# Optimization experiments

Measured on AMD Instinct MI355X. Metric: run time of the kernel, lower is better.

The kernel has to match this reference:

```python
import jax, jax.numpy as jnp
import numpy as np

N = 32768        # batch of sampled sequences
H = 1024         # LSTM hidden (cell) size
P = 128          # proj_size == output_size == operator_length
IN = 2 * (P + 1) + 4 + 1  # 263 = 2*(operator_length+1) + scatter_max_degree + 1
SOFT = 64        # soft_length
TSS = 16.0       # two_sigma_square
AZB, AZE = 0, 32    # operators.arity_zero_begin/end (token layout assumption)
A2B, A2E = 96, 128  # operators.arity_two_begin/end


def setup_inputs() -> dict:
    key = jax.random.key(0)
    ks = jax.random.split(key, 16)
    s = 0.05
    inp = {
        "input": jax.random.normal(ks[0], (N, IN), jnp.float32),
        "hidden": jax.random.normal(ks[1], (2, N, H), jnp.float32),       # c-state
        "hidden_lstm": jax.random.normal(ks[2], (2, N, P), jnp.float32),  # h-state (proj)
        # layer 0 (input -> H, projected to P)
        "W_ih0": jax.random.normal(ks[3], (4 * H, IN), jnp.float32) * s,
        "W_hh0": jax.random.normal(ks[4], (4 * H, P), jnp.float32) * s,
        "b_ih0": jax.random.normal(ks[5], (4 * H,), jnp.float32) * s,
        "b_hh0": jax.random.normal(ks[6], (4 * H,), jnp.float32) * s,
        "W_hr0": jax.random.normal(ks[7], (P, H), jnp.float32) * s,
        # layer 1 (P -> H, projected to P)
        "W_ih1": jax.random.normal(ks[8], (4 * H, P), jnp.float32) * s,
        "W_hh1": jax.random.normal(ks[9], (4 * H, P), jnp.float32) * s,
        "b_ih1": jax.random.normal(ks[10], (4 * H,), jnp.float32) * s,
        "b_hh1": jax.random.normal(ks[11], (4 * H,), jnp.float32) * s,
        "W_hr1": jax.random.normal(ks[12], (P, H), jnp.float32) * s,
        "cur_length": 10,
    }
    return inp


def lstm_cell(x, h, c, Wih, Whh, bih, bhh, Whr):
    # PyTorch gate order: i, f, g, o ; proj_size projection via Whr
    gates = x @ Wih.T + h @ Whh.T + (bih + bhh)   # [n, 4H]
    i, f, g, o = jnp.split(gates, 4, axis=-1)
    c_new = jax.nn.sigmoid(f) * c + jax.nn.sigmoid(i) * jnp.tanh(g)
    h_new = (jax.nn.sigmoid(o) * jnp.tanh(c_new)) @ Whr.T  # project H -> P
    return h_new, c_new


def reference(input, hidden, hidden_lstm,
              W_ih0, W_hh0, b_ih0, b_hh0, W_hr0,
              W_ih1, W_hh1, b_ih1, b_hh1, W_hr1,
              cur_length):
    h0, c0 = lstm_cell(input, hidden_lstm[0], hidden[0], W_ih0, W_hh0, b_ih0, b_hh0, W_hr0)
    h1, c1 = lstm_cell(h0, hidden_lstm[1], hidden[1], W_ih1, W_hh1, b_ih1, b_hh1, W_hr1)
    # prior bias (cur_length is a static Python int)
    prior = jnp.zeros((P,), jnp.float32)
    if cur_length < SOFT:
        prior = prior.at[AZB:AZE].set(-float(SOFT - cur_length) ** 2 / TSS)
    elif cur_length > SOFT:
        prior = prior.at[A2B:A2E].set(-float(cur_length - SOFT) ** 2 / TSS)
    out = jax.nn.softmax(h1 + prior[None, :], axis=1)  # [n, P]
    cn = jnp.stack([c0, c1])  # [2, n, H]
    hn = jnp.stack([h0, h1])  # [2, n, P]
    return out, cn, hn
```

## Files before the change

### kernel.cpp

```cpp
#include <hip/hip_runtime.h>
#include <stdint.h>

#define NB 32768
#define HH 1024
#define PP 128
#define INW 263
#define K0P 448
#define K1P 256
#define G4H 4096

typedef __attribute__((ext_vector_type(8))) short short8;
typedef __attribute__((ext_vector_type(4))) float floatx4;

__device__ __forceinline__ unsigned short f2bf(float x) {
    union { float f; unsigned int u; } v; v.f = x;
    unsigned int r = v.u + 0x7fffu + ((v.u >> 16) & 1u);
    return (unsigned short)(r >> 16);
}
__device__ __forceinline__ float sigm(float x) { return 1.f / (1.f + __expf(-x)); }
__device__ __forceinline__ float tanhfast(float x) { return 2.f / (1.f + __expf(-2.f * x)) - 1.f; }

__device__ __forceinline__ void load_lds16(const void* g, void* l) {
    __builtin_amdgcn_global_load_lds((const __attribute__((address_space(1))) void*)g,
                                     (__attribute__((address_space(3))) void*)l,
                                     16, 0, 0);
}

__global__ void prep_inputs(const float* __restrict__ inp, const float* __restrict__ hl,
                            unsigned short* __restrict__ X0, unsigned short* __restrict__ X1) {
    const int T0 = NB * K0P;
    const int T1 = T0 + NB * PP;
    for (int idx = blockIdx.x * 256 + threadIdx.x; idx < T1; idx += gridDim.x * 256) {
        if (idx < T0) {
            int n = idx / K0P, c = idx - n * K0P;
            float v = 0.f;
            if (c < INW) v = inp[n * INW + c];
            else if (c < INW + PP) v = hl[n * PP + (c - INW)];
            X0[idx] = f2bf(v);
        } else {
            int k = idx - T0;
            int n = k >> 7, c = k & 127;
            X1[n * K1P + PP + c] = f2bf(hl[NB * PP + k]);
        }
    }
}

__global__ void prep_weights(const float* __restrict__ Wih0, const float* __restrict__ Whh0,
                             const float* __restrict__ Wih1, const float* __restrict__ Whh1,
                             const float* __restrict__ Whr0, const float* __restrict__ Whr1,
                             const float* __restrict__ bih0, const float* __restrict__ bhh0,
                             const float* __restrict__ bih1, const float* __restrict__ bhh1,
                             unsigned short* __restrict__ Wp0, unsigned short* __restrict__ Wp1,
                             unsigned short* __restrict__ Whr0b, unsigned short* __restrict__ Whr1b,
                             float* __restrict__ b0, float* __restrict__ b1) {
    const int T0 = G4H * K0P;
    const int T1 = T0 + G4H * K1P;
    const int T2 = T1 + PP * HH;
    const int T3 = T2 + PP * HH;
    const int T4 = T3 + G4H;
    const int T5 = T4 + G4H;
    for (int idx = blockIdx.x * 256 + threadIdx.x; idx < T5; idx += gridDim.x * 256) {
        if (idx < T0) {
            int r = idx / K0P, c = idx - r * K0P;
            int cbb = r >> 7, tt = r & 127;
            int src = (tt >> 5) * 1024 + cbb * 32 + (tt & 31);
            float v = 0.f;
            if (c < INW) v = Wih0[src * INW + c];
            else if (c < INW + PP) v = Whh0[src * PP + (c - INW)];
            Wp0[idx] = f2bf(v);
        } else if (idx < T1) {
            int k = idx - T0;
            int r = k >> 8, c = k & 255;
            int cbb = r >> 7, tt = r & 127;
            int src = (tt >> 5) * 1024 + cbb * 32 + (tt & 31);
            float v = (c < PP) ? Wih1[src * PP + c] : Whh1[src * PP + (c - PP)];
            Wp1[k] = f2bf(v);
        } else if (idx < T2) {
            int k = idx - T1; Whr0b[k] = f2bf(Whr0[k]);
        } else if (idx < T3) {
            int k = idx - T2; Whr1b[k] = f2bf(Whr1[k]);
        } else if (idx < T4) {
            int k = idx - T3; b0[k] = bih0[k] + bhh0[k];
        } else {
            int k = idx - T4; b1[k] = bih1[k] + bhh1[k];
        }
    }
}

template<int KPAD>
__global__ __launch_bounds__(256, 2) void gemm_gates_k(
    const unsigned short* __restrict__ A,
    const unsigned short* __restrict__ Bp,
    const float* __restrict__ bias,
    const float* __restrict__ c_prev,
    float* __restrict__ c_out,
    unsigned short* __restrict__ tmp_out)
{
    __shared__ unsigned short As[128 * 64];
    __shared__ unsigned short Bs[128 * 64];
    const int t  = threadIdx.x;
    const int w  = t >> 6;
    const int l  = t & 63;
    const int lc = l & 15;
    const int q4 = l >> 4;
    const int cb = blockIdx.x;
    const int mb = blockIdx.y;

    floatx4 acc[2][8];
#pragma unroll
    for (int i = 0; i < 2; ++i)
#pragma unroll
        for (int j = 0; j < 8; ++j) acc[i][j] = (floatx4){0.f, 0.f, 0.f, 0.f};

    const int arow = t >> 3;
    const int sw   = ((t & 7) ^ ((t >> 3) & 7)) * 8;
    const unsigned short* gA = A  + (size_t)(mb * 128 + arow) * KPAD + sw;
    const unsigned short* gB = Bp + (size_t)(cb * 128 + arow) * KPAD + sw;
    char* ldsA = (char*)As + t * 16;
    char* ldsB = (char*)Bs + t * 16;

    for (int kt = 0; kt < KPAD; kt += 64) {
#pragma unroll
        for (int i = 0; i < 4; ++i) {
            load_lds16(gA + (size_t)(i * 32) * KPAD + kt, ldsA + i * 4096);
            load_lds16(gB + (size_t)(i * 32) * KPAD + kt, ldsB + i * 4096);
        }
        __syncthreads();
        const short* Asp = (const short*)As;
        const short* Bsp = (const short*)Bs;
#pragma unroll
        for (int kc = 0; kc < 2; ++kc) {
            const int kchunk = kc * 4 + q4;
            const int rsw = (kchunk ^ (lc & 7)) * 8;
            short8 a[2];
#pragma unroll
            for (int mi = 0; mi < 2; ++mi)
                a[mi] = *(const short8*)&Asp[(w * 32 + mi * 16 + lc) * 64 + rsw];
#pragma unroll
            for (int ci = 0; ci < 8; ++ci) {
                short8 b = *(const short8*)&Bsp[(ci * 16 + lc) * 64 + rsw];
#pragma unroll
                for (int mi = 0; mi < 2; ++mi)
                    acc[mi][ci] = __builtin_amdgcn_mfma_f32_16x16x32_bf16(a[mi], b, acc[mi][ci], 0, 0, 0);
            }
        }
        __syncthreads();
    }

#pragma unroll
    for (int u4 = 0; u4 < 2; ++u4) {
        const int hidx = cb * 32 + u4 * 16 + lc;
        const float bi = bias[hidx];
        const float bf = bias[1024 + hidx];
        const float bg = bias[2048 + hidx];
        const float bo = bias[3072 + hidx];
#pragma unroll
        for (int mi = 0; mi < 2; ++mi) {
#pragma unroll
            for (int r = 0; r < 4; ++r) {
                const int row = mb * 128 + w * 32 + mi * 16 + q4 * 4 + r;
                const float iv = acc[mi][0 + u4][r] + bi;
                const float fv = acc[mi][2 + u4][r] + bf;
                const float gv = acc[mi][4 + u4][r] + bg;
                const float ov = acc[mi][6 + u4][r] + bo;
                const float cp = c_prev[(size_t)row * 1024 + hidx];
                const float cn = sigm(fv) * cp + sigm(iv) * tanhfast(gv);
                c_out[(size_t)row * 1024 + hidx] = cn;
                tmp_out[(size_t)row * 1024 + hidx] = f2bf(sigm(ov) * tanhfast(cn));
            }
        }
    }
}

__global__ __launch_bounds__(256, 2) void gemm_proj_k(
    const unsigned short* __restrict__ A,
    const unsigned short* __restrict__ B,
    float* __restrict__ hout,
    unsigned short* __restrict__ xc1)
{
    __shared__ unsigned short As[128 * 64];
    __shared__ unsigned short Bs[128 * 64];
    const int t  = threadIdx.x;
    const int w  = t >> 6;
    const int l  = t & 63;
    const int lc = l & 15;
    const int q4 = l >> 4;
    const int mb = blockIdx.x;

    floatx4 acc[2][8];
#pragma unroll
    for (int i = 0; i < 2; ++i)
#pragma unroll
        for (int j = 0; j < 8; ++j) acc[i][j] = (floatx4){0.f, 0.f, 0.f, 0.f};

    const int arow = t >> 3;
    const int sw   = ((t & 7) ^ ((t >> 3) & 7)) * 8;
    const unsigned short* gA = A + (size_t)(mb * 128 + arow) * 1024 + sw;
    const unsigned short* gB = B + (size_t)arow * 1024 + sw;
    char* ldsA = (char*)As + t * 16;
    char* ldsB = (char*)Bs + t * 16;

    for (int kt = 0; kt < 1024; kt += 64) {
#pragma unroll
        for (int i = 0; i < 4; ++i) {
            load_lds16(gA + (size_t)(i * 32) * 1024 + kt, ldsA + i * 4096);
            load_lds16(gB + (size_t)(i * 32) * 1024 + kt, ldsB + i * 4096);
        }
        __syncthreads();
        const short* Asp = (const short*)As;
        const short* Bsp = (const short*)Bs;
#pragma unroll
        for (int kc = 0; kc < 2; ++kc) {
            const int kchunk = kc * 4 + q4;
            const int rsw = (kchunk ^ (lc & 7)) * 8;
            short8 a[2];
#pragma unroll
            for (int mi = 0; mi < 2; ++mi)
                a[mi] = *(const short8*)&Asp[(w * 32 + mi * 16 + lc) * 64 + rsw];
#pragma unroll
            for (int ci = 0; ci < 8; ++ci) {
                short8 b = *(const short8*)&Bsp[(ci * 16 + lc) * 64 + rsw];
#pragma unroll
                for (int mi = 0; mi < 2; ++mi)
                    acc[mi][ci] = __builtin_amdgcn_mfma_f32_16x16x32_bf16(a[mi], b, acc[mi][ci], 0, 0, 0);
            }
        }
        __syncthreads();
    }

#pragma unroll
    for (int ci = 0; ci < 8; ++ci) {
        const int col = ci * 16 + lc;
#pragma unroll
        for (int mi = 0; mi < 2; ++mi) {
#pragma unroll
            for (int r = 0; r < 4; ++r) {
                const int row = mb * 128 + w * 32 + mi * 16 + q4 * 4 + r;
                const float v = acc[mi][ci][r];
                hout[(size_t)row * 128 + col] = v;
                if (xc1) xc1[(size_t)row * K1P + col] = f2bf(v);
            }
        }
    }
}

__global__ void softmax_k(const float* __restrict__ h1, const int* __restrict__ clp,
                          float* __restrict__ out) {
    const int w = threadIdx.x >> 6, l = threadIdx.x & 63;
    const int row = blockIdx.x * 4 + w;
    const int cl = clp[0];
    float pd = 0.f;
    float d = (float)(64 - cl);
    float pv = -(d * d) * (1.f / 16.f);
    float p0 = (cl < 64 && l < 32) ? pv : 0.f;
    float p1 = (cl > 64 && (l + 64) >= 96) ? pv : 0.f;
    (void)pd;
    float v0 = h1[(size_t)row * 128 + l] + p0;
    float v1 = h1[(size_t)row * 128 + 64 + l] + p1;
    float m = fmaxf(v0, v1);
#pragma unroll
    for (int off = 32; off > 0; off >>= 1) m = fmaxf(m, __shfl_xor(m, off, 64));
    float e0 = __expf(v0 - m), e1 = __expf(v1 - m);
    float s = e0 + e1;
#pragma unroll
    for (int off = 32; off > 0; off >>= 1) s += __shfl_xor(s, off, 64);
    float inv = 1.f / s;
    out[(size_t)row * 128 + l] = e0 * inv;
    out[(size_t)row * 128 + 64 + l] = e1 * inv;
}

extern "C" void kernel_launch(void* const* d_in, const int* in_sizes, int n_in,
                              void* d_out, int out_size, void* d_ws, size_t ws_size,
                              hipStream_t stream) {
    const float* input = (const float*)d_in[0];
    const float* hidden = (const float*)d_in[1];
    const float* hlstm  = (const float*)d_in[2];
    const float* Wih0 = (const float*)d_in[3];
    const float* Whh0 = (const float*)d_in[4];
    const float* bih0 = (const float*)d_in[5];
    const float* bhh0 = (const float*)d_in[6];
    const float* Whr0 = (const float*)d_in[7];
    const float* Wih1 = (const float*)d_in[8];
    const float* Whh1 = (const float*)d_in[9];
    const float* bih1 = (const float*)d_in[10];
    const float* bhh1 = (const float*)d_in[11];
    const float* Whr1 = (const float*)d_in[12];
    const int* curlen = (const int*)d_in[13];

    float* out = (float*)d_out;
    float* cn0 = out + (size_t)NB * PP;
    float* cn1 = cn0 + (size_t)NB * HH;
    float* hn0 = cn1 + (size_t)NB * HH;
    float* hn1 = hn0 + (size_t)NB * PP;

    char* p = (char*)d_ws;
    unsigned short* X0    = (unsigned short*)p; p += (size_t)NB * K0P * 2;
    unsigned short* X1    = (unsigned short*)p; p += (size_t)NB * K1P * 2;
    unsigned short* Wp0   = (unsigned short*)p; p += (size_t)G4H * K0P * 2;
    unsigned short* Wp1   = (unsigned short*)p; p += (size_t)G4H * K1P * 2;
    unsigned short* Whr0b = (unsigned short*)p; p += (size_t)PP * HH * 2;
    unsigned short* Whr1b = (unsigned short*)p; p += (size_t)PP * HH * 2;
    float* b0 = (float*)p; p += (size_t)G4H * 4;
    float* b1 = (float*)p; p += (size_t)G4H * 4;
    unsigned short* tmp0 = (unsigned short*)p; p += (size_t)NB * HH * 2;
    unsigned short* tmp1 = (unsigned short*)p; p += (size_t)NB * HH * 2;

    prep_inputs<<<8192, 256, 0, stream>>>(input, hlstm, X0, X1);
    prep_weights<<<4096, 256, 0, stream>>>(Wih0, Whh0, Wih1, Whh1, Whr0, Whr1,
                                           bih0, bhh0, bih1, bhh1,
                                           Wp0, Wp1, Whr0b, Whr1b, b0, b1);
    gemm_gates_k<K0P><<<dim3(32, 256), 256, 0, stream>>>(X0, Wp0, b0, hidden, cn0, tmp0);
    gemm_proj_k<<<256, 256, 0, stream>>>(tmp0, Whr0b, hn0, X1);
    gemm_gates_k<K1P><<<dim3(32, 256), 256, 0, stream>>>(X1, Wp1, b1, hidden + (size_t)NB * HH, cn1, tmp1);
    gemm_proj_k<<<256, 256, 0, stream>>>(tmp1, Whr1b, hn1, nullptr);
    softmax_k<<<NB / 4, 256, 0, stream>>>(hn1, curlen, out);
}
```

Baseline: 913.8 us.

## Double-buffer LDS tiles and prefetch c_prev/bias before GEMM main loop

Both GEMM kernels now use two LDS buffers per operand, issuing the global-to-LDS loads for the next K tile before computing the current one. Manual vmcnt waits and raw barriers replace the __syncthreads pairs. The gates kernel also loads c_prev and the bias values into registers before the main loop, hiding their latency behind the MFMA work. This doubles LDS use to 64KB per block, which may limit occupancy at 2 blocks/CU, and adds 40 live registers for the prefetched values.

```diff
diff --git a/kernel.cpp b/kernel.cpp
--- a/kernel.cpp
+++ b/kernel.cpp
@@ -96,8 +96,8 @@
     float* __restrict__ c_out,
     unsigned short* __restrict__ tmp_out)
 {
-    __shared__ unsigned short As[128 * 64];
-    __shared__ unsigned short Bs[128 * 64];
+    __shared__ unsigned short As[2 * 128 * 64];
+    __shared__ unsigned short Bs[2 * 128 * 64];
     const int t  = threadIdx.x;
     const int w  = t >> 6;
     const int l  = t & 63;
@@ -112,22 +112,60 @@
 #pragma unroll
         for (int j = 0; j < 8; ++j) acc[i][j] = (floatx4){0.f, 0.f, 0.f, 0.f};
 
+    float cpv[2][2][4];
+    float bv[2][4];
+#pragma unroll
+    for (int u4 = 0; u4 < 2; ++u4) {
+        const int hidx = cb * 32 + u4 * 16 + lc;
+#pragma unroll
+        for (int j = 0; j < 4; ++j) bv[u4][j] = bias[j * 1024 + hidx];
+#pragma unroll
+        for (int mi = 0; mi < 2; ++mi)
+#pragma unroll
+            for (int r = 0; r < 4; ++r)
+                cpv[u4][mi][r] =
+                    c_prev[(size_t)(mb * 128 + w * 32 + mi * 16 + q4 * 4 + r) * 1024 + hidx];
+    }
+    asm volatile("" ::: "memory");
+
     const int arow = t >> 3;
     const int sw   = ((t & 7) ^ ((t >> 3) & 7)) * 8;
     const unsigned short* gA = A  + (size_t)(mb * 128 + arow) * KPAD + sw;
     const unsigned short* gB = Bp + (size_t)(cb * 128 + arow) * KPAD + sw;
-    char* ldsA = (char*)As + t * 16;
-    char* ldsB = (char*)Bs + t * 16;
-
-    for (int kt = 0; kt < KPAD; kt += 64) {
+
+    constexpr int NT = KPAD / 64;
+
+    {
+        char* lA = (char*)As + t * 16;
+        char* lB = (char*)Bs + t * 16;
 #pragma unroll
         for (int i = 0; i < 4; ++i) {
-            load_lds16(gA + (size_t)(i * 32) * KPAD + kt, ldsA + i * 4096);
-            load_lds16(gB + (size_t)(i * 32) * KPAD + kt, ldsB + i * 4096);
-        }
-        __syncthreads();
-        const short* Asp = (const short*)As;
-        const short* Bsp = (const short*)Bs;
+            load_lds16(gA + (size_t)(i * 32) * KPAD, lA + i * 4096);
+            load_lds16(gB + (size_t)(i * 32) * KPAD, lB + i * 4096);
+        }
+    }
+
+#pragma unroll
+    for (int ki = 0; ki < NT; ++ki) {
+        const int cur = ki & 1;
+        if (ki + 1 < NT) {
+            const int kt = (ki + 1) * 64;
+            char* lA = (char*)As + (cur ^ 1) * 16384 + t * 16;
+            char* lB = (char*)Bs + (cur ^ 1) * 16384 + t * 16;
+#pragma unroll
+            for (int i = 0; i < 4; ++i) {
+                load_lds16(gA + (size_t)(i * 32) * KPAD + kt, lA + i * 4096);
+                load_lds16(gB + (size_t)(i * 32) * KPAD + kt, lB + i * 4096);
+            }
+            asm volatile("s_waitcnt vmcnt(8)" ::: "memory");
+        } else {
+            asm volatile("s_waitcnt vmcnt(0)" ::: "memory");
+        }
+        __builtin_amdgcn_s_barrier();
+        asm volatile("" ::: "memory");
+
+        const short* Asp = (const short*)As + cur * 8192;
+        const short* Bsp = (const short*)Bs + cur * 8192;
 #pragma unroll
         for (int kc = 0; kc < 2; ++kc) {
             const int kchunk = kc * 4 + q4;
@@ -144,16 +182,20 @@
                     acc[mi][ci] = __builtin_amdgcn_mfma_f32_16x16x32_bf16(a[mi], b, acc[mi][ci], 0, 0, 0);
             }
         }
-        __syncthreads();
+        if (ki + 1 < NT) {
+            asm volatile("" ::: "memory");
+            __builtin_amdgcn_s_barrier();
+            asm volatile("" ::: "memory");
+        }
     }
 
 #pragma unroll
     for (int u4 = 0; u4 < 2; ++u4) {
         const int hidx = cb * 32 + u4 * 16 + lc;
-        const float bi = bias[hidx];
-        const float bf = bias[1024 + hidx];
-        const float bg = bias[2048 + hidx];
-        const float bo = bias[3072 + hidx];
+        const float bi = bv[u4][0];
+        const float bf = bv[u4][1];
+        const float bg = bv[u4][2];
+        const float bo = bv[u4][3];
 #pragma unroll
         for (int mi = 0; mi < 2; ++mi) {
 #pragma unroll
@@ -163,7 +205,7 @@
                 const float fv = acc[mi][2 + u4][r] + bf;
                 const float gv = acc[mi][4 + u4][r] + bg;
                 const float ov = acc[mi][6 + u4][r] + bo;
-                const float cp = c_prev[(size_t)row * 1024 + hidx];
+                const float cp = cpv[u4][mi][r];
                 const float cn = sigm(fv) * cp + sigm(iv) * tanhfast(gv);
                 c_out[(size_t)row * 1024 + hidx] = cn;
                 tmp_out[(size_t)row * 1024 + hidx] = f2bf(sigm(ov) * tanhfast(cn));
@@ -178,8 +220,8 @@
     float* __restrict__ hout,
     unsigned short* __restrict__ xc1)
 {
-    __shared__ unsigned short As[128 * 64];
-    __shared__ unsigned short Bs[128 * 64];
+    __shared__ unsigned short As[2 * 128 * 64];
+    __shared__ unsigned short Bs[2 * 128 * 64];
     const int t  = threadIdx.x;
     const int w  = t >> 6;
     const int l  = t & 63;
@@ -197,18 +239,40 @@
     const int sw   = ((t & 7) ^ ((t >> 3) & 7)) * 8;
     const unsigned short* gA = A + (size_t)(mb * 128 + arow) * 1024 + sw;
     const unsigned short* gB = B + (size_t)arow * 1024 + sw;
-    char* ldsA = (char*)As + t * 16;
-    char* ldsB = (char*)Bs + t * 16;
-
-    for (int kt = 0; kt < 1024; kt += 64) {
+
+    constexpr int NT = 1024 / 64;
+
+    {
+        char* lA = (char*)As + t * 16;
+        char* lB = (char*)Bs + t * 16;
 #pragma unroll
         for (int i = 0; i < 4; ++i) {
-            load_lds16(gA + (size_t)(i * 32) * 1024 + kt, ldsA + i * 4096);
-            load_lds16(gB + (size_t)(i * 32) * 1024 + kt, ldsB + i * 4096);
-        }
-        __syncthreads();
-        const short* Asp = (const short*)As;
-        const short* Bsp = (const short*)Bs;
+            load_lds16(gA + (size_t)(i * 32) * 1024, lA + i * 4096);
+            load_lds16(gB + (size_t)(i * 32) * 1024, lB + i * 4096);
+        }
+    }
+
+#pragma unroll
+    for (int ki = 0; ki < NT; ++ki) {
+        const int cur = ki & 1;
+        if (ki + 1 < NT) {
+            const int kt = (ki + 1) * 64;
+            char* lA = (char*)As + (cur ^ 1) * 16384 + t * 16;
+            char* lB = (char*)Bs + (cur ^ 1) * 16384 + t * 16;
+#pragma unroll
+            for (int i = 0; i < 4; ++i) {
+                load_lds16(gA + (size_t)(i * 32) * 1024 + kt, lA + i * 4096);
+                load_lds16(gB + (size_t)(i * 32) * 1024 + kt, lB + i * 4096);
+            }
+            asm volatile("s_waitcnt vmcnt(8)" ::: "memory");
+        } else {
+            asm volatile("s_waitcnt vmcnt(0)" ::: "memory");
+        }
+        __builtin_amdgcn_s_barrier();
+        asm volatile("" ::: "memory");
+
+        const short* Asp = (const short*)As + cur * 8192;
+        const short* Bsp = (const short*)Bs + cur * 8192;
 #pragma unroll
         for (int kc = 0; kc < 2; ++kc) {
             const int kchunk = kc * 4 + q4;
@@ -225,7 +289,11 @@
                     acc[mi][ci] = __builtin_amdgcn_mfma_f32_16x16x32_bf16(a[mi], b, acc[mi][ci], 0, 0, 0);
             }
         }
-        __syncthreads();
+        if (ki + 1 < NT) {
+            asm volatile("" ::: "memory");
+            __builtin_amdgcn_s_barrier();
+            asm volatile("" ::: "memory");
+        }
     }
 
 #pragma unroll
```

Measured after the change: 909.4 us. About the same (-0.5%).
